# Kernel tuning notes

Measured on AMD Instinct MI355X. Metric: run time of the kernel, lower is better.

The kernel has to match this reference:

```python
import jax, jax.numpy as jnp
import numpy as np

H, DK = 16, 64
D = H * DK  # d_model = 1024
B, S = 2, 2048


def setup_inputs() -> dict:
    key = jax.random.key(0)
    ks = jax.random.split(key, 11)
    std = 1.0 / np.sqrt(D)
    inp = {
        "query": jax.random.normal(ks[0], (B, S, D), dtype=jnp.float32),
        "key": jax.random.normal(ks[1], (B, S, D), dtype=jnp.float32),
        "value": jax.random.normal(ks[2], (B, S, D), dtype=jnp.float32),
        "Wq": jax.random.normal(ks[3], (D, D), dtype=jnp.float32) * std,
        "bq": jnp.zeros((D,), dtype=jnp.float32),
        "Wk": jax.random.normal(ks[4], (D, D), dtype=jnp.float32) * std,
        "bk": jnp.zeros((D,), dtype=jnp.float32),
        "Wv": jax.random.normal(ks[5], (D, D), dtype=jnp.float32) * std,
        "bv": jnp.zeros((D,), dtype=jnp.float32),
        "Wo": jax.random.normal(ks[6], (D, D), dtype=jnp.float32) * std,
        "bo": jnp.zeros((D,), dtype=jnp.float32),
    }
    return inp


def reference(query, key, value, Wq, bq, Wk, bk, Wv, bv, Wo, bo):
    # torch.nn.Linear convention: y = x @ W.T + b
    def split_heads(x):
        b, s, _ = x.shape
        return x.reshape(b, s, H, DK).transpose(0, 2, 1, 3)  # [B,H,S,DK]

    q = split_heads(query @ Wq.T + bq)
    k = split_heads(key @ Wk.T + bk)
    v = split_heads(value @ Wv.T + bv)

    scale = 1.0 / jnp.sqrt(jnp.asarray(DK, dtype=q.dtype))
    scores = jnp.einsum("bhqd,bhkd->bhqk", q, k) * scale  # [B,H,S,S]
    p_attn = jax.nn.softmax(scores, axis=-1)
    ctx = jnp.einsum("bhqk,bhkd->bhqd", p_attn, v)  # [B,H,S,DK]

    ctx = ctx.transpose(0, 2, 1, 3).reshape(query.shape[0], -1, H * DK)
    return ctx @ Wo.T + bo
```

## Files before the change

### kernel.cpp

```cpp
#include <hip/hip_runtime.h>
#include <stdint.h>

#define BATCH 2
#define SEQ   2048
#define NHEAD 16
#define DK    64
#define DMODEL 1024
#define MROWS (BATCH*SEQ)

typedef __attribute__((ext_vector_type(8))) __bf16 bf16x8;
typedef __attribute__((ext_vector_type(4))) float f32x4;
typedef __attribute__((ext_vector_type(8))) unsigned short u16x8;
typedef __attribute__((ext_vector_type(4))) unsigned short u16x4;
typedef __attribute__((ext_vector_type(4))) unsigned int u32x4;

__device__ __forceinline__ unsigned short f2bf(float f) {
  union { float f; uint32_t u; } c; c.f = f;
  uint32_t u = c.u;
  return (unsigned short)((u + 0x7fffu + ((u >> 16) & 1u)) >> 16);
}

__device__ __forceinline__ void gld16(const void* g, void* lds) {
  __builtin_amdgcn_global_load_lds(
      (const __attribute__((address_space(1))) void*)g,
      (__attribute__((address_space(3))) void*)lds,
      16, 0, 0);
}

__device__ __forceinline__ void cvt_body(const float* __restrict__ in,
                                         unsigned short* __restrict__ out) {
  int i = (blockIdx.x * 256 + threadIdx.x) * 8;
  float4 a = *(const float4*)(in + i);
  float4 b = *(const float4*)(in + i + 4);
  u16x8 o;
  o[0]=f2bf(a.x); o[1]=f2bf(a.y); o[2]=f2bf(a.z); o[3]=f2bf(a.w);
  o[4]=f2bf(b.x); o[5]=f2bf(b.y); o[6]=f2bf(b.z); o[7]=f2bf(b.w);
  *(u16x8*)(out + i) = o;
}

__global__ __launch_bounds__(256)
void cvt3(const float* __restrict__ a, const float* __restrict__ b, const float* __restrict__ c,
          unsigned short* __restrict__ oa, unsigned short* __restrict__ ob,
          unsigned short* __restrict__ oc) {
  int y = blockIdx.y;
  const float* in = (y == 0) ? a : (y == 1) ? b : c;
  unsigned short* out = (y == 0) ? oa : (y == 1) ? ob : oc;
  cvt_body(in, out);
}

__global__ __launch_bounds__(256)
void cvt4(const float* __restrict__ a, const float* __restrict__ b, const float* __restrict__ c,
          const float* __restrict__ d,
          unsigned short* __restrict__ oa, unsigned short* __restrict__ ob,
          unsigned short* __restrict__ oc, unsigned short* __restrict__ od) {
  int y = blockIdx.y;
  const float* in = (y == 0) ? a : (y == 1) ? b : (y == 2) ? c : d;
  unsigned short* out = (y == 0) ? oa : (y == 1) ? ob : (y == 2) ? oc : od;
  cvt_body(in, out);
}

__device__ __forceinline__ void gemm_body(const unsigned short* __restrict__ X,
                                          const unsigned short* __restrict__ W,
                                          const float* __restrict__ bias,
                                          unsigned short* __restrict__ Yb,
                                          float* __restrict__ Yf,
                                          int mode) {
  __shared__ unsigned short lA[128 * 64];
  __shared__ unsigned short lB[128 * 64];
  const int t = threadIdx.x;
  const int lane = t & 63, wave = t >> 6;
  const int cl = lane & 15, qd = lane >> 4;
  const int wm = wave >> 1, wn = wave & 1;
  const int rowBase = blockIdx.y * 128;
  const int colBase = blockIdx.x * 128;
  const int srow = t >> 3, sslot = t & 7;

  f32x4 zero = {0.f, 0.f, 0.f, 0.f};
  f32x4 acc[4][4];
  for (int mt = 0; mt < 4; mt++) for (int nt = 0; nt < 4; nt++) acc[mt][nt] = zero;

  for (int k0 = 0; k0 < DMODEL; k0 += 64) {
    __syncthreads();
    #pragma unroll
    for (int i = 0; i < 4; i++) {
      int r = i * 32 + srow;
      int chunk = sslot ^ (r & 7);
      gld16(X + (size_t)(rowBase + r) * DMODEL + k0 + chunk * 8,
            (char*)lA + i * 4096 + wave * 1024);
      gld16(W + (size_t)(colBase + r) * DMODEL + k0 + chunk * 8,
            (char*)lB + i * 4096 + wave * 1024);
    }
    __syncthreads();
    #pragma unroll
    for (int ks = 0; ks < 2; ks++) {
      bf16x8 af[4], bfr[4];
      #pragma unroll
      for (int mt = 0; mt < 4; mt++) {
        int r = wm * 64 + mt * 16 + cl;
        int slot = (ks * 4 + qd) ^ (r & 7);
        af[mt] = *(const bf16x8*)&lA[r * 64 + slot * 8];
      }
      #pragma unroll
      for (int nt = 0; nt < 4; nt++) {
        int r = wn * 64 + nt * 16 + cl;
        int slot = (ks * 4 + qd) ^ (r & 7);
        bfr[nt] = *(const bf16x8*)&lB[r * 64 + slot * 8];
      }
      #pragma unroll
      for (int mt = 0; mt < 4; mt++)
        #pragma unroll
        for (int nt = 0; nt < 4; nt++)
          acc[mt][nt] = __builtin_amdgcn_mfma_f32_16x16x32_bf16(af[mt], bfr[nt], acc[mt][nt], 0, 0, 0);
    }
  }
  if (mode == 2) {
    #pragma unroll
    for (int mt = 0; mt < 4; mt++) {
      int row0 = rowBase + wm * 64 + mt * 16 + qd * 4;
      int bb = row0 >> 11;
      int s_in = row0 & 2047;
      int blk = s_in & ~63;
      int n4 = (s_in & 63) >> 2;
      int l4 = n4 & 7;
      int pos = 8 * (n4 >> 3) + ((l4 < 4) ? 2 * l4 : 2 * (l4 - 4) + 1);
      #pragma unroll
      for (int nt = 0; nt < 4; nt++) {
        int c = colBase + wn * 64 + nt * 16 + cl;
        float bv = bias[c];
        int hh = c >> 6, d = c & 63;
        u16x4 v;
        #pragma unroll
        for (int r = 0; r < 4; r++) v[r] = f2bf(acc[mt][nt][r] + bv);
        *(u16x4*)&Yb[(size_t)((bb * NHEAD + hh) * 64 + d) * SEQ + blk + pos * 4] = v;
      }
    }
  } else {
    #pragma unroll
    for (int mt = 0; mt < 4; mt++) {
      int row = rowBase + wm * 64 + mt * 16 + qd * 4;
      #pragma unroll
      for (int nt = 0; nt < 4; nt++) {
        int c = colBase + wn * 64 + nt * 16 + cl;
        float bv = bias[c];
        #pragma unroll
        for (int r = 0; r < 4; r++) {
          float v = acc[mt][nt][r] + bv;
          if (mode == 3)      Yf[(size_t)(row + r) * DMODEL + c] = v;
          else if (mode == 1) Yb[(size_t)(row + r) * DMODEL + c] = f2bf(v * 0.125f);
          else                Yb[(size_t)(row + r) * DMODEL + c] = f2bf(v);
        }
      }
    }
  }
}

__global__ __launch_bounds__(256)
void gemm_qkv(const unsigned short* __restrict__ Xq, const unsigned short* __restrict__ Xk,
              const unsigned short* __restrict__ Xv,
              const unsigned short* __restrict__ Wq, const unsigned short* __restrict__ Wk,
              const unsigned short* __restrict__ Wv,
              const float* __restrict__ bq, const float* __restrict__ bk,
              const float* __restrict__ bv,
              unsigned short* __restrict__ Q, unsigned short* __restrict__ K,
              unsigned short* __restrict__ VT) {
  int z = blockIdx.z;
  const unsigned short* X = (z == 0) ? Xq : (z == 1) ? Xk : Xv;
  const unsigned short* W = (z == 0) ? Wq : (z == 1) ? Wk : Wv;
  const float* b = (z == 0) ? bq : (z == 1) ? bk : bv;
  unsigned short* Y = (z == 0) ? Q : (z == 1) ? K : VT;
  int mode = (z == 0) ? 1 : (z == 1) ? 0 : 2;
  gemm_body(X, W, b, Y, nullptr, mode);
}

__global__ __launch_bounds__(256)
void gemm_out(const unsigned short* __restrict__ CTX, const unsigned short* __restrict__ Wo,
              const float* __restrict__ bo, float* __restrict__ out) {
  gemm_body(CTX, Wo, bo, nullptr, out, 3);
}

__global__ __launch_bounds__(256)
void attn(const unsigned short* __restrict__ Q, const unsigned short* __restrict__ K,
          const unsigned short* __restrict__ VT, unsigned short* __restrict__ CTX) {
  __shared__ unsigned short lK[64 * 64];
  __shared__ unsigned short lV[64 * 64];
  const int t = threadIdx.x, lane = t & 63, wave = t >> 6;
  const int cl = lane & 15, qd = lane >> 4;
  const int qt = blockIdx.x, h = blockIdx.y, b = blockIdx.z;
  const int srow = t >> 3, sslot = t & 7;

  #pragma unroll
  for (int i = 0; i < 2; i++) {
    int r = i * 32 + srow;
    int chunk = sslot ^ (r & 7);
    gld16(Q + (size_t)(b * SEQ + qt * 64 + r) * DMODEL + h * 64 + chunk * 8,
          (char*)lK + i * 4096 + wave * 1024);
  }
  __syncthreads();
  bf16x8 qf[2];
  #pragma unroll
  for (int ks = 0; ks < 2; ks++) {
    int r = wave * 16 + cl;
    int slot = (ks * 4 + qd) ^ (r & 7);
    qf[ks] = *(const bf16x8*)&lK[r * 64 + slot * 8];
  }

  f32x4 zero = {0.f, 0.f, 0.f, 0.f};
  f32x4 o[4];
  #pragma unroll
  for (int dt = 0; dt < 4; dt++) o[dt] = zero;
  float rsum = 0.f;

  for (int kt = 0; kt < SEQ / 64; kt++) {
    __syncthreads();
    #pragma unroll
    for (int i = 0; i < 2; i++) {
      int r = i * 32 + srow;
      int chunk = sslot ^ (r & 7);
      gld16(K + (size_t)(b * SEQ + kt * 64 + r) * DMODEL + h * 64 + chunk * 8,
            (char*)lK + i * 4096 + wave * 1024);
      gld16(VT + (size_t)((b * NHEAD + h) * 64 + r) * SEQ + kt * 64 + chunk * 8,
            (char*)lV + i * 4096 + wave * 1024);
    }
    __syncthreads();

    f32x4 sc[4];
    #pragma unroll
    for (int nt = 0; nt < 4; nt++) sc[nt] = zero;
    #pragma unroll
    for (int ks = 0; ks < 2; ks++)
      #pragma unroll
      for (int nt = 0; nt < 4; nt++) {
        int rk = nt * 16 + cl;
        int slot = (ks * 4 + qd) ^ (rk & 7);
        bf16x8 kf = *(const bf16x8*)&lK[rk * 64 + slot * 8];
        sc[nt] = __builtin_amdgcn_mfma_f32_16x16x32_bf16(kf, qf[ks], sc[nt], 0, 0, 0);
      }

    float p[4][4];
    #pragma unroll
    for (int nt = 0; nt < 4; nt++)
      #pragma unroll
      for (int r = 0; r < 4; r++) {
        float v = __expf(sc[nt][r]);
        p[nt][r] = v; rsum += v;
      }

    #pragma unroll
    for (int ntp = 0; ntp < 2; ntp++) {
      bf16x8 pb;
      #pragma unroll
      for (int j = 0; j < 4; j++) pb[j] = (__bf16)p[2 * ntp][j];
      #pragma unroll
      for (int j = 0; j < 4; j++) pb[4 + j] = (__bf16)p[2 * ntp + 1][j];
      #pragma unroll
      for (int dt = 0; dt < 4; dt++) {
        int d = dt * 16 + cl;
        int slot = (4 * ntp + qd) ^ (d & 7);
        bf16x8 vf = *(const bf16x8*)&lV[d * 64 + slot * 8];
        o[dt] = __builtin_amdgcn_mfma_f32_16x16x32_bf16(vf, pb, o[dt], 0, 0, 0);
      }
    }
  }

  rsum += __shfl_xor(rsum, 16, 64);
  rsum += __shfl_xor(rsum, 32, 64);
  float inv = 1.f / rsum;

  int row = b * SEQ + qt * 64 + wave * 16 + cl;
  #pragma unroll
  for (int dt = 0; dt < 4; dt++) {
    u16x4 v;
    #pragma unroll
    for (int r = 0; r < 4; r++) v[r] = f2bf(o[dt][r] * inv);
    *(u16x4*)&CTX[(size_t)row * DMODEL + h * 64 + dt * 16 + qd * 4] = v;
  }
}

extern "C" void kernel_launch(void* const* d_in, const int* in_sizes, int n_in,
                              void* d_out, int out_size, void* d_ws, size_t ws_size,
                              hipStream_t stream) {
  const float* q  = (const float*)d_in[0];
  const float* k  = (const float*)d_in[1];
  const float* v  = (const float*)d_in[2];
  const float* Wq = (const float*)d_in[3]; const float* bq = (const float*)d_in[4];
  const float* Wk = (const float*)d_in[5]; const float* bk = (const float*)d_in[6];
  const float* Wv = (const float*)d_in[7]; const float* bv = (const float*)d_in[8];
  const float* Wo = (const float*)d_in[9]; const float* bo = (const float*)d_in[10];
  float* out = (float*)d_out;

  char* ws = (char*)d_ws;
  const size_t MB = 1u << 20;
  unsigned short* Xq  = (unsigned short*)(ws + 0 * MB);
  unsigned short* Xk  = (unsigned short*)(ws + 8 * MB);
  unsigned short* Xv  = (unsigned short*)(ws + 16 * MB);
  unsigned short* Wqb = (unsigned short*)(ws + 24 * MB);
  unsigned short* Wkb = (unsigned short*)(ws + 26 * MB);
  unsigned short* Wvb = (unsigned short*)(ws + 28 * MB);
  unsigned short* Wob = (unsigned short*)(ws + 30 * MB);
  unsigned short* Qp  = (unsigned short*)(ws + 32 * MB);
  unsigned short* Kp  = (unsigned short*)(ws + 40 * MB);
  unsigned short* VT  = (unsigned short*)(ws + 48 * MB);
  unsigned short* CTX = (unsigned short*)(ws + 56 * MB);

  const int nX = MROWS * DMODEL;
  const int nW = DMODEL * DMODEL;
  cvt3<<<dim3(nX / 2048, 3), 256, 0, stream>>>(q, k, v, Xq, Xk, Xv);
  cvt4<<<dim3(nW / 2048, 4), 256, 0, stream>>>(Wq, Wk, Wv, Wo, Wqb, Wkb, Wvb, Wob);

  gemm_qkv<<<dim3(DMODEL / 128, MROWS / 128, 3), 256, 0, stream>>>(
      Xq, Xk, Xv, Wqb, Wkb, Wvb, bq, bk, bv, Qp, Kp, VT);

  attn<<<dim3(SEQ / 64, NHEAD, BATCH), 256, 0, stream>>>(Qp, Kp, VT, CTX);

  gemm_out<<<dim3(DMODEL / 128, MROWS / 128), 256, 0, stream>>>(CTX, Wob, bo, out);
}
```

Baseline: 239.4 us.

## Double-buffer K/V, process two query tiles per block, use exp2, merge conversions

The attention kernel now handles 128 query rows per block as two groups, so each K/V tile loaded into LDS feeds twice as many MFMAs. K/V loads are double-buffered so the next tile is fetched while the current one is computed. The Q scale is folded to include log2(e) so the kernel can use the native exp2 instruction. The two conversion kernels are merged into one launch. The kernel still uses no running max (no stabilisation), same as before. The grid halves to 512 blocks, which lowers occupancy, and register pressure rises.

```diff
diff --git a/kernel.cpp b/kernel.cpp
--- a/kernel.cpp
+++ b/kernel.cpp
@@ -14,6 +14,8 @@
 typedef __attribute__((ext_vector_type(4))) unsigned short u16x4;
 typedef __attribute__((ext_vector_type(4))) unsigned int u32x4;
 
+#define QSCALE 0.18033688f
+
 __device__ __forceinline__ unsigned short f2bf(float f) {
   union { float f; uint32_t u; } c; c.f = f;
   uint32_t u = c.u;
@@ -27,36 +29,34 @@
       16, 0, 0);
 }
 
-__device__ __forceinline__ void cvt_body(const float* __restrict__ in,
-                                         unsigned short* __restrict__ out) {
-  int i = (blockIdx.x * 256 + threadIdx.x) * 8;
+__global__ __launch_bounds__(256)
+void cvt_all(const float* __restrict__ q, const float* __restrict__ k, const float* __restrict__ v,
+             const float* __restrict__ Wq, const float* __restrict__ Wk,
+             const float* __restrict__ Wv, const float* __restrict__ Wo,
+             unsigned short* __restrict__ Xq, unsigned short* __restrict__ Xk,
+             unsigned short* __restrict__ Xv,
+             unsigned short* __restrict__ Wqb, unsigned short* __restrict__ Wkb,
+             unsigned short* __restrict__ Wvb, unsigned short* __restrict__ Wob) {
+  int blk = blockIdx.x;
+  const float* in; unsigned short* out; int base;
+  if (blk < 6144) {
+    int ti = blk >> 11;
+    in  = (ti == 0) ? q  : (ti == 1) ? k  : v;
+    out = (ti == 0) ? Xq : (ti == 1) ? Xk : Xv;
+    base = (blk & 2047) * 2048;
+  } else {
+    int ti = (blk - 6144) >> 9;
+    in  = (ti == 0) ? Wq  : (ti == 1) ? Wk  : (ti == 2) ? Wv  : Wo;
+    out = (ti == 0) ? Wqb : (ti == 1) ? Wkb : (ti == 2) ? Wvb : Wob;
+    base = ((blk - 6144) & 511) * 2048;
+  }
+  int i = base + threadIdx.x * 8;
   float4 a = *(const float4*)(in + i);
   float4 b = *(const float4*)(in + i + 4);
   u16x8 o;
   o[0]=f2bf(a.x); o[1]=f2bf(a.y); o[2]=f2bf(a.z); o[3]=f2bf(a.w);
   o[4]=f2bf(b.x); o[5]=f2bf(b.y); o[6]=f2bf(b.z); o[7]=f2bf(b.w);
   *(u16x8*)(out + i) = o;
-}
-
-__global__ __launch_bounds__(256)
-void cvt3(const float* __restrict__ a, const float* __restrict__ b, const float* __restrict__ c,
-          unsigned short* __restrict__ oa, unsigned short* __restrict__ ob,
-          unsigned short* __restrict__ oc) {
-  int y = blockIdx.y;
-  const float* in = (y == 0) ? a : (y == 1) ? b : c;
-  unsigned short* out = (y == 0) ? oa : (y == 1) ? ob : oc;
-  cvt_body(in, out);
-}
-
-__global__ __launch_bounds__(256)
-void cvt4(const float* __restrict__ a, const float* __restrict__ b, const float* __restrict__ c,
-          const float* __restrict__ d,
-          unsigned short* __restrict__ oa, unsigned short* __restrict__ ob,
-          unsigned short* __restrict__ oc, unsigned short* __restrict__ od) {
-  int y = blockIdx.y;
-  const float* in = (y == 0) ? a : (y == 1) ? b : (y == 2) ? c : d;
-  unsigned short* out = (y == 0) ? oa : (y == 1) ? ob : (y == 2) ? oc : od;
-  cvt_body(in, out);
 }
 
 __device__ __forceinline__ void gemm_body(const unsigned short* __restrict__ X,
@@ -146,7 +146,7 @@
         for (int r = 0; r < 4; r++) {
           float v = acc[mt][nt][r] + bv;
           if (mode == 3)      Yf[(size_t)(row + r) * DMODEL + c] = v;
-          else if (mode == 1) Yb[(size_t)(row + r) * DMODEL + c] = f2bf(v * 0.125f);
+          else if (mode == 1) Yb[(size_t)(row + r) * DMODEL + c] = f2bf(v * QSCALE);
           else                Yb[(size_t)(row + r) * DMODEL + c] = f2bf(v);
         }
       }
@@ -181,98 +181,128 @@
 __global__ __launch_bounds__(256)
 void attn(const unsigned short* __restrict__ Q, const unsigned short* __restrict__ K,
           const unsigned short* __restrict__ VT, unsigned short* __restrict__ CTX) {
-  __shared__ unsigned short lK[64 * 64];
-  __shared__ unsigned short lV[64 * 64];
+  __shared__ unsigned short lK[2][64 * 64];
+  __shared__ unsigned short lV[2][64 * 64];
   const int t = threadIdx.x, lane = t & 63, wave = t >> 6;
   const int cl = lane & 15, qd = lane >> 4;
   const int qt = blockIdx.x, h = blockIdx.y, b = blockIdx.z;
   const int srow = t >> 3, sslot = t & 7;
 
   #pragma unroll
+  for (int half = 0; half < 2; half++)
+    #pragma unroll
+    for (int i = 0; i < 2; i++) {
+      int r = i * 32 + srow;
+      int chunk = sslot ^ (r & 7);
+      gld16(Q + (size_t)(b * SEQ + qt * 128 + half * 64 + r) * DMODEL + h * 64 + chunk * 8,
+            (char*)lK[half] + i * 4096 + wave * 1024);
+    }
+  __syncthreads();
+  bf16x8 qf[2][2];
+  #pragma unroll
+  for (int qg = 0; qg < 2; qg++)
+    #pragma unroll
+    for (int ks = 0; ks < 2; ks++) {
+      int r = wave * 16 + cl;
+      int slot = (ks * 4 + qd) ^ (r & 7);
+      qf[qg][ks] = *(const bf16x8*)&lK[qg][r * 64 + slot * 8];
+    }
+  __syncthreads();
+
+  #pragma unroll
   for (int i = 0; i < 2; i++) {
     int r = i * 32 + srow;
     int chunk = sslot ^ (r & 7);
-    gld16(Q + (size_t)(b * SEQ + qt * 64 + r) * DMODEL + h * 64 + chunk * 8,
-          (char*)lK + i * 4096 + wave * 1024);
-  }
-  __syncthreads();
-  bf16x8 qf[2];
-  #pragma unroll
-  for (int ks = 0; ks < 2; ks++) {
-    int r = wave * 16 + cl;
-    int slot = (ks * 4 + qd) ^ (r & 7);
-    qf[ks] = *(const bf16x8*)&lK[r * 64 + slot * 8];
+    gld16(K + (size_t)(b * SEQ + r) * DMODEL + h * 64 + chunk * 8,
+          (char*)lK[0] + i * 4096 + wave * 1024);
+    gld16(VT + (size_t)((b * NHEAD + h) * 64 + r) * SEQ + chunk * 8,
+          (char*)lV[0] + i * 4096 + wave * 1024);
   }
 
   f32x4 zero = {0.f, 0.f, 0.f, 0.f};
-  f32x4 o[4];
-  #pragma unroll
-  for (int dt = 0; dt < 4; dt++) o[dt] = zero;
-  float rsum = 0.f;
+  f32x4 o[2][4];
+  #pragma unroll
+  for (int qg = 0; qg < 2; qg++)
+    #pragma unroll
+    for (int dt = 0; dt < 4; dt++) o[qg][dt] = zero;
+  float rsum[2] = {0.f, 0.f};
 
   for (int kt = 0; kt < SEQ / 64; kt++) {
+    const int c = kt & 1;
     __syncthreads();
-    #pragma unroll
-    for (int i = 0; i < 2; i++) {
-      int r = i * 32 + srow;
-      int chunk = sslot ^ (r & 7);
-      gld16(K + (size_t)(b * SEQ + kt * 64 + r) * DMODEL + h * 64 + chunk * 8,
-            (char*)lK + i * 4096 + wave * 1024);
-      gld16(VT + (size_t)((b * NHEAD + h) * 64 + r) * SEQ + kt * 64 + chunk * 8,
-            (char*)lV + i * 4096 + wave * 1024);
-    }
-    __syncthreads();
-
-    f32x4 sc[4];
-    #pragma unroll
-    for (int nt = 0; nt < 4; nt++) sc[nt] = zero;
+    if (kt + 1 < SEQ / 64) {
+      #pragma unroll
+      for (int i = 0; i < 2; i++) {
+        int r = i * 32 + srow;
+        int chunk = sslot ^ (r & 7);
+        gld16(K + (size_t)(b * SEQ + (kt + 1) * 64 + r) * DMODEL + h * 64 + chunk * 8,
+              (char*)lK[c ^ 1] + i * 4096 + wave * 1024);
+        gld16(VT + (size_t)((b * NHEAD + h) * 64 + r) * SEQ + (kt + 1) * 64 + chunk * 8,
+              (char*)lV[c ^ 1] + i * 4096 + wave * 1024);
+      }
+    }
+
+    f32x4 sc[2][4];
+    #pragma unroll
+    for (int qg = 0; qg < 2; qg++)
+      #pragma unroll
+      for (int nt = 0; nt < 4; nt++) sc[qg][nt] = zero;
     #pragma unroll
     for (int ks = 0; ks < 2; ks++)
       #pragma unroll
       for (int nt = 0; nt < 4; nt++) {
         int rk = nt * 16 + cl;
         int slot = (ks * 4 + qd) ^ (rk & 7);
-        bf16x8 kf = *(const bf16x8*)&lK[rk * 64 + slot * 8];
-        sc[nt] = __builtin_amdgcn_mfma_f32_16x16x32_bf16(kf, qf[ks], sc[nt], 0, 0, 0);
-      }
-
-    float p[4][4];
-    #pragma unroll
-    for (int nt = 0; nt < 4; nt++)
-      #pragma unroll
-      for (int r = 0; r < 4; r++) {
-        float v = __expf(sc[nt][r]);
-        p[nt][r] = v; rsum += v;
-      }
-
-    #pragma unroll
-    for (int ntp = 0; ntp < 2; ntp++) {
-      bf16x8 pb;
-      #pragma unroll
-      for (int j = 0; j < 4; j++) pb[j] = (__bf16)p[2 * ntp][j];
-      #pragma unroll
-      for (int j = 0; j < 4; j++) pb[4 + j] = (__bf16)p[2 * ntp + 1][j];
+        bf16x8 kf = *(const bf16x8*)&lK[c][rk * 64 + slot * 8];
+        sc[0][nt] = __builtin_amdgcn_mfma_f32_16x16x32_bf16(kf, qf[0][ks], sc[0][nt], 0, 0, 0);
+        sc[1][nt] = __builtin_amdgcn_mfma_f32_16x16x32_bf16(kf, qf[1][ks], sc[1][nt], 0, 0, 0);
+      }
+
+    bf16x8 pb[2][2];
+    #pragma unroll
+    for (int qg = 0; qg < 2; qg++)
+      #pragma unroll
+      for (int ntp = 0; ntp < 2; ntp++) {
+        bf16x8 x;
+        #pragma unroll
+        for (int j = 0; j < 4; j++) {
+          float v = __builtin_amdgcn_exp2f(sc[qg][2 * ntp][j]);
+          rsum[qg] += v; x[j] = (__bf16)v;
+        }
+        #pragma unroll
+        for (int j = 0; j < 4; j++) {
+          float v = __builtin_amdgcn_exp2f(sc[qg][2 * ntp + 1][j]);
+          rsum[qg] += v; x[4 + j] = (__bf16)v;
+        }
+        pb[qg][ntp] = x;
+      }
+
+    #pragma unroll
+    for (int ntp = 0; ntp < 2; ntp++)
       #pragma unroll
       for (int dt = 0; dt < 4; dt++) {
         int d = dt * 16 + cl;
         int slot = (4 * ntp + qd) ^ (d & 7);
-        bf16x8 vf = *(const bf16x8*)&lV[d * 64 + slot * 8];
-        o[dt] = __builtin_amdgcn_mfma_f32_16x16x32_bf16(vf, pb, o[dt], 0, 0, 0);
-      }
-    }
-  }
-
-  rsum += __shfl_xor(rsum, 16, 64);
-  rsum += __shfl_xor(rsum, 32, 64);
-  float inv = 1.f / rsum;
-
-  int row = b * SEQ + qt * 64 + wave * 16 + cl;
-  #pragma unroll
-  for (int dt = 0; dt < 4; dt++) {
-    u16x4 v;
-    #pragma unroll
-    for (int r = 0; r < 4; r++) v[r] = f2bf(o[dt][r] * inv);
-    *(u16x4*)&CTX[(size_t)row * DMODEL + h * 64 + dt * 16 + qd * 4] = v;
+        bf16x8 vf = *(const bf16x8*)&lV[c][d * 64 + slot * 8];
+        o[0][dt] = __builtin_amdgcn_mfma_f32_16x16x32_bf16(vf, pb[0][ntp], o[0][dt], 0, 0, 0);
+        o[1][dt] = __builtin_amdgcn_mfma_f32_16x16x32_bf16(vf, pb[1][ntp], o[1][dt], 0, 0, 0);
+      }
+  }
+
+  #pragma unroll
+  for (int qg = 0; qg < 2; qg++) {
+    float rs = rsum[qg];
+    rs += __shfl_xor(rs, 16, 64);
+    rs += __shfl_xor(rs, 32, 64);
+    float inv = 1.f / rs;
+    int row = b * SEQ + qt * 128 + qg * 64 + wave * 16 + cl;
+    #pragma unroll
+    for (int dt = 0; dt < 4; dt++) {
+      u16x4 v;
+      #pragma unroll
+      for (int r = 0; r < 4; r++) v[r] = f2bf(o[qg][dt][r] * inv);
+      *(u16x4*)&CTX[(size_t)row * DMODEL + h * 64 + dt * 16 + qd * 4] = v;
+    }
   }
 }
 
@@ -302,15 +332,13 @@
   unsigned short* VT  = (unsigned short*)(ws + 48 * MB);
   unsigned short* CTX = (unsigned short*)(ws + 56 * MB);
 
-  const int nX = MROWS * DMODEL;
-  const int nW = DMODEL * DMODEL;
-  cvt3<<<dim3(nX / 2048, 3), 256, 0, stream>>>(q, k, v, Xq, Xk, Xv);
-  cvt4<<<dim3(nW / 2048, 4), 256, 0, stream>>>(Wq, Wk, Wv, Wo, Wqb, Wkb, Wvb, Wob);
+  cvt_all<<<8192, 256, 0, stream>>>(q, k, v, Wq, Wk, Wv, Wo,
+                                    Xq, Xk, Xv, Wqb, Wkb, Wvb, Wob);
 
   gemm_qkv<<<dim3(DMODEL / 128, MROWS / 128, 3), 256, 0, stream>>>(
       Xq, Xk, Xv, Wqb, Wkb, Wvb, bq, bk, bv, Qp, Kp, VT);
 
-  attn<<<dim3(SEQ / 64, NHEAD, BATCH), 256, 0, stream>>>(Qp, Kp, VT, CTX);
+  attn<<<dim3(SEQ / 128, NHEAD, BATCH), 256, 0, stream>>>(Qp, Kp, VT, CTX);
 
   gemm_out<<<dim3(DMODEL / 128, MROWS / 128), 256, 0, stream>>>(CTX, Wob, bo, out);
 }
```

Result: no change. 235.9 us (-1.5%).
